# Kernel optimization log

Hardware: AMD Instinct MI355X
Metric: run time of the kernel (lower is better)

The kernel has to match this reference:

```python
import jax, jax.numpy as jnp
import numpy as np


def _dequantize(qweight, scale, zero_point, bits, group_size):
    """Unpack int32-packed weights and apply group-wise dequantization.

    qweight:    [N, K // (32//bits)] int32, value i within an int32 at shift i*bits
    scale/zp:   [N, K // group_size]
    returns W:  [N, K] float32
    """
    vpi = 32 // bits  # values per int32
    mask = (1 << bits) - 1
    N, packed = qweight.shape
    K = packed * vpi
    shifts = (jnp.arange(vpi, dtype=jnp.int32) * bits)  # [vpi]
    # [N, packed, vpi] -> flatten so value i of each int32 lands at consecutive K positions
    q = (qweight[:, :, None] >> shifts[None, None, :]) & mask
    q = q.reshape(N, K // group_size, group_size).astype(jnp.float32)
    w = scale[:, :, None] * (q - zero_point[:, :, None])  # group-wise dequant
    return w.reshape(N, K)


def setup_inputs() -> dict:
    key = jax.random.key(0)
    k1, k2, k3, k4, k5 = jax.random.split(key, 5)
    B, S, K, N = 4, 2048, 4096, 4096
    bits, group_size = 4, 128
    vpi = 32 // bits
    num_groups = K // group_size
    x = jax.random.normal(k1, (B, S, K), dtype=jnp.float32)
    qweight = jax.random.randint(k2, (N, K // vpi), jnp.iinfo(jnp.int32).min,
                                 jnp.iinfo(jnp.int32).max, dtype=jnp.int32)
    scale = jax.random.uniform(k3, (N, num_groups), dtype=jnp.float32,
                               minval=0.001, maxval=0.02)
    zero_point = jax.random.uniform(k4, (N, num_groups), dtype=jnp.float32,
                                    minval=0.0, maxval=float((1 << bits) - 1))
    bias = jax.random.normal(k5, (N,), dtype=jnp.float32)
    return {"x": x, "qweight": qweight, "scale": scale, "zero_point": zero_point,
            "bias": bias, "bits": bits, "group_size": group_size}


def reference(x, qweight, scale, zero_point, bias, bits, group_size):
    # Fused dequant + GEMM: y = x @ W^T + b, W dequantized from packed int4 groups
    w = _dequantize(qweight, scale, zero_point, bits, group_size)  # [N, K]
    y = jnp.einsum('bsk,nk->bsn', x, w)
    return y + bias
```

## Files before the change

kernel.cpp:

```cpp
#include <hip/hip_runtime.h>

#define KD 4096
#define ND 4096
#define GRP 32

typedef unsigned short u16;
typedef float   f32x4  __attribute__((ext_vector_type(4)));
typedef __bf16  bf16x8 __attribute__((ext_vector_type(8)));
typedef unsigned short u16x8 __attribute__((ext_vector_type(8)));
typedef unsigned short u16x4 __attribute__((ext_vector_type(4)));

__device__ __forceinline__ u16 f2bf(float f) {
  unsigned u = __float_as_uint(f);
  return (u16)((u + 0x7fffu + ((u >> 16) & 1u)) >> 16);
}

__device__ __forceinline__ void async16(const void* g, void* l) {
  __builtin_amdgcn_global_load_lds(
      (const __attribute__((address_space(1))) unsigned int*)g,
      (__attribute__((address_space(3))) unsigned int*)l, 16, 0, 0);
}

__global__ __launch_bounds__(256) void dequant_w_kernel(
    const int* __restrict__ qw, const float* __restrict__ scale,
    const float* __restrict__ zp, u16* __restrict__ wout) {
  int idx = blockIdx.x * 256 + threadIdx.x;
  int n = idx >> 9;
  int p = idx & 511;
  int g = p >> 4;
  float s = scale[n * GRP + g];
  float b = -s * zp[n * GRP + g];
  unsigned q = (unsigned)qw[idx];
  u16x8 hv;
#pragma unroll
  for (int i = 0; i < 8; ++i) {
    float f = fmaf((float)((q >> (4 * i)) & 15u), s, b);
    hv[i] = f2bf(f);
  }
  *(u16x8*)(wout + (size_t)idx * 8) = hv;
}

__global__ __launch_bounds__(256) void convert_x_kernel(
    const float4* __restrict__ x, u16x4* __restrict__ o, int n4) {
  int i = blockIdx.x * 256 + threadIdx.x;
  int stride = gridDim.x * 256;
  for (; i < n4; i += stride) {
    float4 v = x[i];
    u16x4 h;
    h[0] = f2bf(v.x); h[1] = f2bf(v.y); h[2] = f2bf(v.z); h[3] = f2bf(v.w);
    o[i] = h;
  }
}

template <int XF32, int WQ>
__global__ __launch_bounds__(256, 3) void gemm_kernel(
    const u16*   __restrict__ xb,
    const float* __restrict__ xf,
    const u16*   __restrict__ wb,
    const int*   __restrict__ qw,
    const float* __restrict__ scale,
    const float* __restrict__ zp,
    const float* __restrict__ bias,
    float* __restrict__ out) {
  __shared__ u16 As[128 * 32];
  __shared__ u16 Bs[128 * 32];
  const int tid = threadIdx.x;
  const int l = tid & 63, w = tid >> 6;
  const int m0 = blockIdx.y * 128, n0 = blockIdx.x * 128;
  const int wm = (w >> 1) * 64, wn = (w & 1) * 64;
  const int col = l & 15, quad = l >> 4;
  f32x4 acc[4][4] = {};

  for (int k0 = 0; k0 < KD; k0 += 32) {
    __syncthreads();

    if constexpr (XF32) {
#pragma unroll
      for (int it = 0; it < 4; ++it) {
        int fi = it * 256 + tid;
        int row = fi >> 3, cs = fi & 7;
        float4 v = *(const float4*)(xf + (size_t)(m0 + row) * KD + k0 + cs * 4);
        u16x4 h;
        h[0] = f2bf(v.x); h[1] = f2bf(v.y); h[2] = f2bf(v.z); h[3] = f2bf(v.w);
        *(u16x4*)(&As[row * 32 + cs * 4]) = h;
      }
    } else {
#pragma unroll
      for (int c = 0; c < 2; ++c) {
        int br = (w * 2 + c) * 16;
        const u16* g = xb + (size_t)(m0 + br + (l >> 2)) * KD + k0 + (l & 3) * 8;
        async16(g, &As[br * 32]);
      }
    }

    if constexpr (WQ) {
#pragma unroll
      for (int it = 0; it < 2; ++it) {
        int qi = it * 256 + tid;
        int row = qi >> 2, p4 = qi & 3;
        int nrow = n0 + row;
        int g = k0 >> 7;
        float s = scale[nrow * GRP + g];
        float b = -s * zp[nrow * GRP + g];
        unsigned q = (unsigned)qw[(size_t)nrow * (KD / 8) + (k0 >> 3) + p4];
        u16x8 hv;
#pragma unroll
        for (int i = 0; i < 8; ++i) {
          float f = fmaf((float)((q >> (4 * i)) & 15u), s, b);
          hv[i] = f2bf(f);
        }
        *(u16x8*)(&Bs[row * 32 + p4 * 8]) = hv;
      }
    } else {
#pragma unroll
      for (int c = 0; c < 2; ++c) {
        int br = (w * 2 + c) * 16;
        const u16* g = wb + (size_t)(n0 + br + (l >> 2)) * KD + k0 + (l & 3) * 8;
        async16(g, &Bs[br * 32]);
      }
    }

    __syncthreads();

    bf16x8 a[4], b[4];
#pragma unroll
    for (int i = 0; i < 4; ++i)
      a[i] = *(const bf16x8*)&As[(wm + i * 16 + col) * 32 + quad * 8];
#pragma unroll
    for (int j = 0; j < 4; ++j)
      b[j] = *(const bf16x8*)&Bs[(wn + j * 16 + col) * 32 + quad * 8];
#pragma unroll
    for (int i = 0; i < 4; ++i)
#pragma unroll
      for (int j = 0; j < 4; ++j)
        acc[i][j] = __builtin_amdgcn_mfma_f32_16x16x32_bf16(a[i], b[j], acc[i][j], 0, 0, 0);
  }

#pragma unroll
  for (int j = 0; j < 4; ++j) {
    int n = n0 + wn + j * 16 + col;
    float bj = bias[n];
#pragma unroll
    for (int i = 0; i < 4; ++i) {
      int mrow = m0 + wm + i * 16 + quad * 4;
#pragma unroll
      for (int r = 0; r < 4; ++r)
        out[(size_t)(mrow + r) * ND + n] = acc[i][j][r] + bj;
    }
  }
}

extern "C" void kernel_launch(void* const* d_in, const int* in_sizes, int n_in,
                              void* d_out, int out_size, void* d_ws, size_t ws_size,
                              hipStream_t stream) {
  const float* x     = (const float*)d_in[0];
  const int*   qw    = (const int*)d_in[1];
  const float* scale = (const float*)d_in[2];
  const float* zp    = (const float*)d_in[3];
  const float* bias  = (const float*)d_in[4];
  float* out = (float*)d_out;

  const int M = in_sizes[0] / KD;
  dim3 grid(ND / 128, M / 128), block(256);

  const size_t needW = (size_t)ND * KD * sizeof(u16);
  const size_t needX = (size_t)M * KD * sizeof(u16);

  if (ws_size >= needW + needX) {
    u16* wb = (u16*)d_ws;
    u16* xb = wb + (size_t)ND * KD;
    dequant_w_kernel<<<(ND * (KD / 8)) / 256, 256, 0, stream>>>(qw, scale, zp, wb);
    convert_x_kernel<<<4096, 256, 0, stream>>>((const float4*)x, (u16x4*)xb, M * KD / 4);
    gemm_kernel<0, 0><<<grid, block, 0, stream>>>(xb, x, wb, qw, scale, zp, bias, out);
  } else if (ws_size >= needW) {
    u16* wb = (u16*)d_ws;
    dequant_w_kernel<<<(ND * (KD / 8)) / 256, 256, 0, stream>>>(qw, scale, zp, wb);
    gemm_kernel<1, 0><<<grid, block, 0, stream>>>(nullptr, x, wb, qw, scale, zp, bias, out);
  } else {
    gemm_kernel<1, 1><<<grid, block, 0, stream>>>(nullptr, x, nullptr, qw, scale, zp, bias, out);
  }
}
```

Before: 546.6 us.

## Swizzle LDS tiles, merge prep kernels, raise GEMM occupancy hint

XOR-swizzles the 16-byte chunk positions in the A and B shared-memory tiles, on both the async global-to-LDS loads and the MFMA operand reads, to reduce LDS bank conflicts. Merges the weight dequant and x-to-bf16 conversion into one launch, with each thread converting 8 x values. Raises the launch-bounds occupancy hint from 3 to 4 blocks per CU, which may force register spilling.

```diff
diff --git a/kernel.cpp b/kernel.cpp
--- a/kernel.cpp
+++ b/kernel.cpp
@@ -21,39 +21,36 @@
       (__attribute__((address_space(3))) unsigned int*)l, 16, 0, 0);
 }
 
-__global__ __launch_bounds__(256) void dequant_w_kernel(
+__global__ __launch_bounds__(256) void prep_kernel(
     const int* __restrict__ qw, const float* __restrict__ scale,
-    const float* __restrict__ zp, u16* __restrict__ wout) {
-  int idx = blockIdx.x * 256 + threadIdx.x;
-  int n = idx >> 9;
-  int p = idx & 511;
-  int g = p >> 4;
-  float s = scale[n * GRP + g];
-  float b = -s * zp[n * GRP + g];
-  unsigned q = (unsigned)qw[idx];
-  u16x8 hv;
+    const float* __restrict__ zp, u16* __restrict__ wout,
+    const float4* __restrict__ x, u16x8* __restrict__ xb) {
+  const int b = blockIdx.x, tid = threadIdx.x;
+  if (b < 8192) {
+    int idx = b * 256 + tid;
+    int n = idx >> 9;
+    int p = idx & 511;
+    int g = p >> 4;
+    float s = scale[n * GRP + g];
+    float bz = -s * zp[n * GRP + g];
+    unsigned q = (unsigned)qw[idx];
+    u16x8 hv;
 #pragma unroll
-  for (int i = 0; i < 8; ++i) {
-    float f = fmaf((float)((q >> (4 * i)) & 15u), s, b);
-    hv[i] = f2bf(f);
-  }
-  *(u16x8*)(wout + (size_t)idx * 8) = hv;
-}
-
-__global__ __launch_bounds__(256) void convert_x_kernel(
-    const float4* __restrict__ x, u16x4* __restrict__ o, int n4) {
-  int i = blockIdx.x * 256 + threadIdx.x;
-  int stride = gridDim.x * 256;
-  for (; i < n4; i += stride) {
-    float4 v = x[i];
-    u16x4 h;
-    h[0] = f2bf(v.x); h[1] = f2bf(v.y); h[2] = f2bf(v.z); h[3] = f2bf(v.w);
-    o[i] = h;
+    for (int i = 0; i < 8; ++i)
+      hv[i] = f2bf(fmaf((float)((q >> (4 * i)) & 15u), s, bz));
+    *(u16x8*)(wout + (size_t)idx * 8) = hv;
+  } else {
+    int i = (b - 8192) * 256 + tid;
+    float4 v0 = x[(size_t)i * 2], v1 = x[(size_t)i * 2 + 1];
+    u16x8 h;
+    h[0] = f2bf(v0.x); h[1] = f2bf(v0.y); h[2] = f2bf(v0.z); h[3] = f2bf(v0.w);
+    h[4] = f2bf(v1.x); h[5] = f2bf(v1.y); h[6] = f2bf(v1.z); h[7] = f2bf(v1.w);
+    xb[i] = h;
   }
 }
 
 template <int XF32, int WQ>
-__global__ __launch_bounds__(256, 3) void gemm_kernel(
+__global__ __launch_bounds__(256, 4) void gemm_kernel(
     const u16*   __restrict__ xb,
     const float* __restrict__ xf,
     const u16*   __restrict__ wb,
@@ -69,6 +66,8 @@
   const int m0 = blockIdx.y * 128, n0 = blockIdx.x * 128;
   const int wm = (w >> 1) * 64, wn = (w & 1) * 64;
   const int col = l & 15, quad = l >> 4;
+  const int swz = (col >> 1) & 3;
+  const int cg = (l & 3) ^ ((l >> 3) & 3);
   f32x4 acc[4][4] = {};
 
   for (int k0 = 0; k0 < KD; k0 += 32) {
@@ -82,13 +81,14 @@
         float4 v = *(const float4*)(xf + (size_t)(m0 + row) * KD + k0 + cs * 4);
         u16x4 h;
         h[0] = f2bf(v.x); h[1] = f2bf(v.y); h[2] = f2bf(v.z); h[3] = f2bf(v.w);
-        *(u16x4*)(&As[row * 32 + cs * 4]) = h;
+        int ch = (cs >> 1) ^ ((row >> 1) & 3);
+        *(u16x4*)(&As[row * 32 + ch * 8 + (cs & 1) * 4]) = h;
       }
     } else {
 #pragma unroll
       for (int c = 0; c < 2; ++c) {
         int br = (w * 2 + c) * 16;
-        const u16* g = xb + (size_t)(m0 + br + (l >> 2)) * KD + k0 + (l & 3) * 8;
+        const u16* g = xb + (size_t)(m0 + br + (l >> 2)) * KD + k0 + cg * 8;
         async16(g, &As[br * 32]);
       }
     }
@@ -101,21 +101,19 @@
         int nrow = n0 + row;
         int g = k0 >> 7;
         float s = scale[nrow * GRP + g];
-        float b = -s * zp[nrow * GRP + g];
+        float bz = -s * zp[nrow * GRP + g];
         unsigned q = (unsigned)qw[(size_t)nrow * (KD / 8) + (k0 >> 3) + p4];
         u16x8 hv;
 #pragma unroll
-        for (int i = 0; i < 8; ++i) {
-          float f = fmaf((float)((q >> (4 * i)) & 15u), s, b);
-          hv[i] = f2bf(f);
-        }
-        *(u16x8*)(&Bs[row * 32 + p4 * 8]) = hv;
+        for (int i = 0; i < 8; ++i)
+          hv[i] = f2bf(fmaf((float)((q >> (4 * i)) & 15u), s, bz));
+        *(u16x8*)(&Bs[row * 32 + ((p4 ^ ((row >> 1) & 3)) * 8)]) = hv;
       }
     } else {
 #pragma unroll
       for (int c = 0; c < 2; ++c) {
         int br = (w * 2 + c) * 16;
-        const u16* g = wb + (size_t)(n0 + br + (l >> 2)) * KD + k0 + (l & 3) * 8;
+        const u16* g = wb + (size_t)(n0 + br + (l >> 2)) * KD + k0 + cg * 8;
         async16(g, &Bs[br * 32]);
       }
     }
@@ -125,10 +123,10 @@
     bf16x8 a[4], b[4];
 #pragma unroll
     for (int i = 0; i < 4; ++i)
-      a[i] = *(const bf16x8*)&As[(wm + i * 16 + col) * 32 + quad * 8];
+      a[i] = *(const bf16x8*)&As[(wm + i * 16 + col) * 32 + (quad ^ swz) * 8];
 #pragma unroll
     for (int j = 0; j < 4; ++j)
-      b[j] = *(const bf16x8*)&Bs[(wn + j * 16 + col) * 32 + quad * 8];
+      b[j] = *(const bf16x8*)&Bs[(wn + j * 16 + col) * 32 + (quad ^ swz) * 8];
 #pragma unroll
     for (int i = 0; i < 4; ++i)
 #pragma unroll
@@ -169,12 +167,13 @@
   if (ws_size >= needW + needX) {
     u16* wb = (u16*)d_ws;
     u16* xb = wb + (size_t)ND * KD;
-    dequant_w_kernel<<<(ND * (KD / 8)) / 256, 256, 0, stream>>>(qw, scale, zp, wb);
-    convert_x_kernel<<<4096, 256, 0, stream>>>((const float4*)x, (u16x4*)xb, M * KD / 4);
+    int conv_blocks = (M * (KD / 8)) / 256;
+    prep_kernel<<<8192 + conv_blocks, 256, 0, stream>>>(
+        qw, scale, zp, wb, (const float4*)x, (u16x8*)xb);
     gemm_kernel<0, 0><<<grid, block, 0, stream>>>(xb, x, wb, qw, scale, zp, bias, out);
   } else if (ws_size >= needW) {
     u16* wb = (u16*)d_ws;
-    dequant_w_kernel<<<(ND * (KD / 8)) / 256, 256, 0, stream>>>(qw, scale, zp, wb);
+    prep_kernel<<<8192, 256, 0, stream>>>(qw, scale, zp, wb, nullptr, nullptr);
     gemm_kernel<1, 0><<<grid, block, 0, stream>>>(nullptr, x, wb, qw, scale, zp, bias, out);
   } else {
     gemm_kernel<1, 1><<<grid, block, 0, stream>>>(nullptr, x, nullptr, qw, scale, zp, bias, out);
```

New measurement: 538.6 us. Within noise of the previous version (-1.5%).
